# Kernel tuning notes

Hardware: AMD Instinct MI355X
Metric: run time of the kernel (lower is better)

The kernel has to match this reference:

```python
import jax, jax.numpy as jnp
import numpy as np

EPS = 1e-5  # torch InstanceNorm1d default


def _instance_norm_lastdim(t):
    # torch InstanceNorm1d applied to (b*h, n, d): normalizes over last axis d
    # per (b, h, n) with biased variance, no affine.
    mu = jnp.mean(t, axis=-1, keepdims=True)
    var = jnp.var(t, axis=-1, keepdims=True)
    return (t - mu) * jax.lax.rsqrt(var + EPS)


def setup_inputs() -> dict:
    key = jax.random.key(0)
    k1, k2, k3, k4 = jax.random.split(key, 4)
    b, n, dim = 4, 8192, 128
    heads, dim_head = 8, 64
    inner = heads * dim_head
    x = jax.random.normal(k1, (b, n, dim), dtype=jnp.float32)
    # nn.Linear(dim, inner*3, bias=False): weight (out, in); we store transposed (in, out)
    w_qkv = jax.random.normal(k2, (dim, inner * 3), dtype=jnp.float32) * (1.0 / np.sqrt(dim))
    w_out = jax.random.normal(k3, (inner, dim), dtype=jnp.float32) * (1.0 / np.sqrt(inner))
    b_out = jax.random.normal(k4, (dim,), dtype=jnp.float32) * 0.01
    return {"x": x, "w_qkv": w_qkv, "w_out": w_out, "b_out": b_out}


def reference(x, w_qkv, w_out, b_out):
    b, n, _ = x.shape
    heads, dim_head = 8, 64
    qkv = x @ w_qkv  # (b, n, 3*inner)
    q, k, v = jnp.split(qkv, 3, axis=-1)

    def to_heads(t):
        return t.reshape(b, n, heads, dim_head).transpose(0, 2, 1, 3)  # b h n d

    q, k, v = to_heads(q), to_heads(k), to_heads(v)
    # galerkin: norm k and v (InstanceNorm over dim_head axis)
    k = _instance_norm_lastdim(k)
    v = _instance_norm_lastdim(v)
    dots = jnp.einsum('bhnd,bhne->bhde', k, v)      # K^T V, small (d x d)
    out = jnp.einsum('bhnd,bhde->bhne', q, dots) * (1.0 / n)
    out = out.transpose(0, 2, 1, 3).reshape(b, n, heads * dim_head)
    return out @ w_out + b_out
```

## Files before the change

kernel.cpp:

```cpp
#include <hip/hip_runtime.h>

#define NN 8192
#define DIM 128

typedef short short8 __attribute__((ext_vector_type(8)));
typedef float f32x4 __attribute__((ext_vector_type(4)));

__device__ __forceinline__ unsigned short f2bf(float f) {
  unsigned int u = __float_as_uint(f);
  u = (u + 0x7FFFu + ((u >> 16) & 1u)) >> 16;
  return (unsigned short)u;
}
__device__ __forceinline__ unsigned int cvtpk(float a, float b) {
  unsigned int r;
  asm("v_cvt_pk_bf16_f32 %0, %1, %2" : "=v"(r) : "v"(a), "v"(b));
  return r;
}
__device__ __forceinline__ void gll16(const void* gsrc, void* ldst) {
  __builtin_amdgcn_global_load_lds(
      (const __attribute__((address_space(1))) unsigned int*)gsrc,
      (__attribute__((address_space(3))) unsigned int*)ldst, 16, 0, 0);
}
#define BAR_LGKM()                                          \
  do {                                                      \
    asm volatile("s_waitcnt lgkmcnt(0)" ::: "memory");      \
    __builtin_amdgcn_sched_barrier(0);                      \
    __builtin_amdgcn_s_barrier();                           \
    __builtin_amdgcn_sched_barrier(0);                      \
  } while (0)
#define BAR_VM()                                            \
  do {                                                      \
    asm volatile("s_waitcnt vmcnt(0)" ::: "memory");        \
    __builtin_amdgcn_sched_barrier(0);                      \
    __builtin_amdgcn_s_barrier();                           \
    __builtin_amdgcn_sched_barrier(0);                      \
  } while (0)

__global__ __launch_bounds__(256) void prep_kernel(const float* __restrict__ x,
                                                   const float* __restrict__ wqkv,
                                                   unsigned char* __restrict__ ximg,
                                                   unsigned char* __restrict__ wimg,
                                                   float* __restrict__ dots) {
  __shared__ __align__(16) unsigned char wb[32768];
  const int t = threadIdx.x;
  const int bx = blockIdx.x;
  if (bx < 1024) {
#pragma unroll
    for (int rep = 0; rep < 2; ++rep) {
      const int idx = bx * 512 + rep * 256 + t;
      const int bt = idx >> 10;
      const int o = (idx & 1023) << 4;
      const int r = o >> 8;
      const int q0 = o & 255;
      const int c0 = (q0 ^ ((r & 7) << 4)) >> 1;
      const float* src = x + ((size_t)(bt >> 7) * NN + (size_t)(bt & 127) * 64 + r) * DIM + c0;
      const float4 v0 = *(const float4*)src;
      const float4 v1 = *(const float4*)(src + 4);
      uint4 u;
      u.x = cvtpk(v0.x, v0.y);
      u.y = cvtpk(v0.z, v0.w);
      u.z = cvtpk(v1.x, v1.y);
      u.w = cvtpk(v1.z, v1.w);
      *(uint4*)(ximg + (size_t)idx * 16) = u;
    }
  } else if (bx < 1032) {
    const int h = bx - 1024;
    const int k = t >> 1;
    const int chalf = t & 1;
    const float* wp = wqkv + (size_t)k * 1536 + (chalf ? (1024 + h * 64) : (512 + h * 64));
    const float4* wp4 = (const float4*)wp;
    const int c0 = chalf * 64;
    float4 wv[16];
    float sum = 0.f;
#pragma unroll
    for (int jj = 0; jj < 16; ++jj) {
      wv[jj] = wp4[jj];
      sum += wv[jj].x + wv[jj].y + wv[jj].z + wv[jj].w;
    }
    const float mean = sum * (1.f / 64.f);
#pragma unroll
    for (int jj = 0; jj < 16; ++jj) {
      const int c = c0 + jj * 4;
      const unsigned int cx0 = (unsigned int)((c + 0) & 7) << 4;
      const unsigned int cx1 = (unsigned int)((c + 1) & 7) << 4;
      const unsigned int cx2 = (unsigned int)((c + 2) & 7) << 4;
      const unsigned int cx3 = (unsigned int)((c + 3) & 7) << 4;
      *(unsigned short*)(wb + (c + 0) * 256 + (((unsigned)(2 * k)) ^ cx0)) = f2bf(wv[jj].x - mean);
      *(unsigned short*)(wb + (c + 1) * 256 + (((unsigned)(2 * k)) ^ cx1)) = f2bf(wv[jj].y - mean);
      *(unsigned short*)(wb + (c + 2) * 256 + (((unsigned)(2 * k)) ^ cx2)) = f2bf(wv[jj].z - mean);
      *(unsigned short*)(wb + (c + 3) * 256 + (((unsigned)(2 * k)) ^ cx3)) = f2bf(wv[jj].w - mean);
    }
    __syncthreads();
    const uint4* s4 = (const uint4*)(wb + t * 128);
    uint4* d4 = (uint4*)(wimg + (size_t)h * 32768 + t * 128);
#pragma unroll
    for (int i = 0; i < 8; ++i) d4[i] = s4[i];
  } else {
    const int zb = bx - 1032;
    float4* dz = (float4*)dots + (size_t)zb * 4096 + t;
    const float4 z = make_float4(0.f, 0.f, 0.f, 0.f);
#pragma unroll
    for (int i = 0; i < 16; ++i) dz[i * 256] = z;
  }
}

__global__ __launch_bounds__(256, 3) void kv_dots_v5(const unsigned char* __restrict__ ximg,
                                                     const unsigned char* __restrict__ wimg,
                                                     float* __restrict__ dots) {
  __shared__ __align__(16) unsigned char smem[49152];
  unsigned char* const WB = smem;

  const int t = threadIdx.x;
  const int bx = blockIdx.x;
  const int h = bx >> 7;
  const int p = bx & 127;
  const int b = p >> 5;
  const int chunk = p & 31;

  const int wave = t >> 6;
  const int lane = t & 63;
  const int lb = lane & 15;
  const int kg = lane >> 4;
  const int g = wave & 1;
  const int ch = wave >> 1;
  const unsigned int lxor = (unsigned int)(lb & 7) << 4;
  const unsigned int rxor = (unsigned int)(lb & 3) << 4;

  const unsigned char* wsrc = wimg + (size_t)h * 32768;
  const unsigned char* xsrc = ximg + (size_t)(b * 128 + chunk * 4) * 16384;

#pragma unroll
  for (int i = 0; i < 8; ++i)
    gll16(wsrc + (i * 4 + wave) * 1024 + lane * 16, WB + (i * 4 + wave) * 1024);

  const int rrow = 16 * g + lb;
  short8 xf[4];
#pragma unroll
  for (int ks = 0; ks < 4; ++ks)
    xf[ks] = *(const short8*)(xsrc + rrow * 256 + (((unsigned)(ks * 64 + kg * 16)) ^ lxor));

  f32x4 dacc[4];
#pragma unroll
  for (int et = 0; et < 4; ++et) dacc[et] = (f32x4)0.f;

  BAR_VM();

  for (int tile = 0; tile < 8; ++tile) {
    short8 xn[4];
    if (tile < 7) {
      const unsigned char* tb = xsrc + (size_t)((tile + 1) >> 1) * 16384 + (size_t)((tile + 1) & 1) * 8192;
#pragma unroll
      for (int ks = 0; ks < 4; ++ks)
        xn[ks] = *(const short8*)(tb + rrow * 256 + (((unsigned)(ks * 64 + kg * 16)) ^ lxor));
    }

    f32x4 acc[4];
#pragma unroll
    for (int ct = 0; ct < 4; ++ct) acc[ct] = (f32x4)0.f;
#pragma unroll
    for (int ks = 0; ks < 4; ++ks) {
      const unsigned int koff = ((unsigned)(ks * 64 + kg * 16)) ^ lxor;
#pragma unroll
      for (int ct = 0; ct < 4; ++ct) {
        const short8 bf = *(const short8*)(WB + (ch * 64 + ct * 16 + lb) * 256 + koff);
        acc[ct] = __builtin_amdgcn_mfma_f32_16x16x32_bf16(xf[ks], bf, acc[ct], 0, 0, 0);
      }
    }

    float sc[4];
#pragma unroll
    for (int e = 0; e < 4; ++e) {
      float s = acc[0][e] * acc[0][e] + acc[1][e] * acc[1][e] +
                acc[2][e] * acc[2][e] + acc[3][e] * acc[3][e];
      s += __shfl_xor(s, 1);
      s += __shfl_xor(s, 2);
      s += __shfl_xor(s, 4);
      s += __shfl_xor(s, 8);
      sc[e] = rsqrtf(s * (1.f / 64.f) + 1e-5f);
    }

    unsigned char* const BUF = smem + 32768 + (tile & 1) * 8192;
    {
      unsigned char* const MYT = BUF + ch * 4096;
      const unsigned int rb = ((unsigned)(g * 32 + kg * 8)) ^ rxor;
#pragma unroll
      for (int ct = 0; ct < 4; ++ct) {
        uint2 w2;
        w2.x = cvtpk(acc[ct][0] * sc[0], acc[ct][1] * sc[1]);
        w2.y = cvtpk(acc[ct][2] * sc[2], acc[ct][3] * sc[3]);
        *(uint2*)(MYT + (ct * 16 + lb) * 64 + rb) = w2;
      }
    }
    BAR_LGKM();

    {
      const unsigned int soff = ((unsigned)(kg * 16)) ^ rxor;
      const short8 a = *(const short8*)(BUF + (wave * 16 + lb) * 64 + soff);
#pragma unroll
      for (int et = 0; et < 4; ++et) {
        const short8 bf = *(const short8*)(BUF + 4096 + (et * 16 + lb) * 64 + soff);
        dacc[et] = __builtin_amdgcn_mfma_f32_16x16x32_bf16(a, bf, dacc[et], 0, 0, 0);
      }
    }

#pragma unroll
    for (int ks = 0; ks < 4; ++ks) xf[ks] = xn[ks];
  }

  float* dp = dots + (size_t)(b * 8 + h) * 4096;
#pragma unroll
  for (int et = 0; et < 4; ++et) {
#pragma unroll
    for (int reg = 0; reg < 4; ++reg) {
      const int d = wave * 16 + kg * 4 + reg;
      const int e = et * 16 + lb;
      atomicAdd(&dp[d * 64 + e], dacc[et][reg]);
    }
  }
}

template <int TR>
__global__ __launch_bounds__(256) void tw_kernel(const float* __restrict__ wqkv,
                                                 const float* __restrict__ wout,
                                                 const float* __restrict__ dots,
                                                 float* __restrict__ part) {
  __shared__ __align__(16) float ds[64 * 66];
  __shared__ __align__(16) float wqT[64 * 36];
  __shared__ __align__(16) float Ts[32 * 66];
  __shared__ __align__(16) float wos[64 * 132];

  const int blk = blockIdx.x;
  const int bh = blk >> 2;
  const int cq = blk & 3;
  const int h = bh & 7;
  const int t = threadIdx.x;

  for (int i = t; i < 4096; i += 256)
    ds[(i >> 6) * 66 + (i & 63)] = dots[(size_t)bh * 4096 + i];

  for (int i = t; i < 2048; i += 256) {
    const int d = i >> 5;
    const int c = i & 31;
    wqT[d * 36 + c] = wqkv[(size_t)(cq * 32 + c) * 1536 + h * 64 + d];
  }

  for (int i = t; i < 2048; i += 256) {
    const int e = i >> 5;
    const int jj = (i & 31) * 4;
    *(float4*)&wos[e * 132 + jj] = *(const float4*)(wout + (size_t)(h * 64 + e) * 128 + jj);
  }
  __syncthreads();

  {
    const int c = t >> 3;
    const int e0 = (t & 7) * 8;
    float acc[8];
#pragma unroll
    for (int q = 0; q < 8; ++q) acc[q] = 0.f;
    for (int d = 0; d < 64; ++d) {
      const float wq = wqT[d * 36 + c];
      const float4 d0 = *(const float4*)&ds[d * 66 + e0];
      const float4 d1 = *(const float4*)&ds[d * 66 + e0 + 4];
      acc[0] += wq * d0.x; acc[1] += wq * d0.y; acc[2] += wq * d0.z; acc[3] += wq * d0.w;
      acc[4] += wq * d1.x; acc[5] += wq * d1.y; acc[6] += wq * d1.z; acc[7] += wq * d1.w;
    }
    *(float4*)&Ts[c * 66 + e0] = make_float4(acc[0], acc[1], acc[2], acc[3]);
    *(float4*)&Ts[c * 66 + e0 + 4] = make_float4(acc[4], acc[5], acc[6], acc[7]);
  }
  __syncthreads();

  {
    const int c = t >> 3;
    const int j0 = (t & 7) * 16;
    float acc[16];
#pragma unroll
    for (int q = 0; q < 16; ++q) acc[q] = 0.f;
    for (int e = 0; e < 64; ++e) {
      const float tv = Ts[c * 66 + e];
#pragma unroll
      for (int q = 0; q < 16; q += 4) {
        const float4 wv = *(const float4*)&wos[e * 132 + j0 + q];
        acc[q + 0] += tv * wv.x;
        acc[q + 1] += tv * wv.y;
        acc[q + 2] += tv * wv.z;
        acc[q + 3] += tv * wv.w;
      }
    }
    if (TR) {
      float* pp = part + (size_t)bh * 16384;
      const int cc = cq * 32 + c;
#pragma unroll
      for (int q = 0; q < 16; ++q) pp[(j0 + q) * 128 + cc] = acc[q];
    } else {
      float* pp = part + (size_t)bh * 16384 + (size_t)(cq * 32 + c) * 128 + j0;
#pragma unroll
      for (int q = 0; q < 16; q += 4)
        *(float4*)&pp[q] = make_float4(acc[q], acc[q + 1], acc[q + 2], acc[q + 3]);
    }
  }
}

__global__ __launch_bounds__(256) void bigw_reduce_v2(const float* __restrict__ part,
                                                      unsigned char* __restrict__ bigwimg) {
  const int idx = blockIdx.x * 256 + threadIdx.x;
  const int b = idx >> 11;
  const int o = (idx & 2047) << 4;
  const int j = o >> 8;
  const int q0 = o & 255;
  const int c0 = (q0 ^ ((j & 7) << 4)) >> 1;
  float s[8];
#pragma unroll
  for (int i = 0; i < 8; ++i) s[i] = 0.f;
  const float* pb = part + (size_t)b * 8 * 16384 + j * 128 + c0;
#pragma unroll
  for (int hh = 0; hh < 8; ++hh) {
    const float4 p0 = *(const float4*)(pb + hh * 16384);
    const float4 p1 = *(const float4*)(pb + hh * 16384 + 4);
    s[0] += p0.x; s[1] += p0.y; s[2] += p0.z; s[3] += p0.w;
    s[4] += p1.x; s[5] += p1.y; s[6] += p1.z; s[7] += p1.w;
  }
  const float inv_n = 1.f / (float)NN;
  uint4 u;
  u.x = cvtpk(s[0] * inv_n, s[1] * inv_n);
  u.y = cvtpk(s[2] * inv_n, s[3] * inv_n);
  u.z = cvtpk(s[4] * inv_n, s[5] * inv_n);
  u.w = cvtpk(s[6] * inv_n, s[7] * inv_n);
  *(uint4*)(bigwimg + (size_t)idx * 16) = u;
}

__global__ __launch_bounds__(256) void out_v2(const unsigned char* __restrict__ ximg,
                                              const unsigned char* __restrict__ bigwimg,
                                              const float* __restrict__ bout,
                                              float* __restrict__ out) {
  __shared__ __align__(16) unsigned char smem[49152];
  unsigned char* const XB = smem;
  unsigned char* const WJ = smem + 16384;

  const int t = threadIdx.x;
  const int bx = blockIdx.x;
  const int b = bx >> 7;
  const int tile = bx & 127;

  const int wave = t >> 6;
  const int lane = t & 63;
  const int lb = lane & 15;
  const int kg = lane >> 4;
  const unsigned int lxor = (unsigned int)(lb & 7) << 4;

  const unsigned char* wsrc = bigwimg + (size_t)b * 32768;
  const unsigned char* xsrc = ximg + (size_t)(b * 128 + tile) * 16384;

#pragma unroll
  for (int i = 0; i < 8; ++i)
    gll16(wsrc + (wave * 8 + i) * 1024 + lane * 16, WJ + (wave * 8 + i) * 1024);
#pragma unroll
  for (int i = 0; i < 4; ++i)
    gll16(xsrc + (wave * 4 + i) * 1024 + lane * 16, XB + (wave * 4 + i) * 1024);

  float bias[8];
#pragma unroll
  for (int ct = 0; ct < 8; ++ct) bias[ct] = bout[ct * 16 + lb];

  BAR_VM();

  f32x4 acc[8];
#pragma unroll
  for (int ct = 0; ct < 8; ++ct) acc[ct] = (f32x4)0.f;
  const int arow = wave * 16 + lb;
#pragma unroll
  for (int ks = 0; ks < 4; ++ks) {
    const unsigned int koff = (unsigned int)(ks * 64 + kg * 16);
    const short8 a = *(const short8*)(XB + arow * 256 + (koff ^ lxor));
#pragma unroll
    for (int ct = 0; ct < 8; ++ct) {
      const short8 bf = *(const short8*)(WJ + (ct * 16 + lb) * 256 + (koff ^ lxor));
      acc[ct] = __builtin_amdgcn_mfma_f32_16x16x32_bf16(a, bf, acc[ct], 0, 0, 0);
    }
  }

  float* op = out + (size_t)(b * NN + tile * 64 + 16 * wave + kg * 4) * DIM;
#pragma unroll
  for (int ct = 0; ct < 8; ++ct) {
#pragma unroll
    for (int reg = 0; reg < 4; ++reg) {
      op[reg * DIM + ct * 16 + lb] = acc[ct][reg] + bias[ct];
    }
  }
}

__global__ __launch_bounds__(256) void zero_dots_fb(float* __restrict__ dots) {
  float4* dz = (float4*)dots + (size_t)blockIdx.x * 4096 + threadIdx.x;
  const float4 z = make_float4(0.f, 0.f, 0.f, 0.f);
#pragma unroll
  for (int i = 0; i < 16; ++i) dz[i * 256] = z;
}

__global__ __launch_bounds__(256) void kv_dots_fb(const float* __restrict__ x,
                                                  const float* __restrict__ wqkv,
                                                  float* __restrict__ dots) {
  __shared__ __align__(16) unsigned char smem[49152];
  unsigned char* const XB = smem;
  unsigned char* const KT = smem;
  unsigned char* const VT = smem + 8192;
  unsigned char* const WB = smem + 16384;

  const int t = threadIdx.x;
  const int bx = blockIdx.x;
  const int h = bx >> 7;
  const int p = bx & 127;
  const int b = p >> 5;
  const int chunk = p & 31;
  const int row0 = chunk * 256;

  const int wave = t >> 6;
  const int lane = t & 63;
  const int lb = lane & 15;
  const int kg = lane >> 4;
  const unsigned int lxor = (unsigned int)(lb & 7) << 4;

  {
    const int k = t >> 1;
    const int chalf = t & 1;
    const float* wp = wqkv + (size_t)k * 1536 + (chalf ? (1024 + h * 64) : (512 + h * 64));
    const float4* wp4 = (const float4*)wp;
    const int c0 = chalf * 64;
    float4 wv[16];
    float sum = 0.f;
#pragma unroll
    for (int jj = 0; jj < 16; ++jj) {
      wv[jj] = wp4[jj];
      sum += wv[jj].x + wv[jj].y + wv[jj].z + wv[jj].w;
    }
    const float mean = sum * (1.f / 64.f);
#pragma unroll
    for (int jj = 0; jj < 16; ++jj) {
      const int c = c0 + jj * 4;
      const unsigned int cx0 = (unsigned int)((c + 0) & 7) << 4;
      const unsigned int cx1 = (unsigned int)((c + 1) & 7) << 4;
      const unsigned int cx2 = (unsigned int)((c + 2) & 7) << 4;
      const unsigned int cx3 = (unsigned int)((c + 3) & 7) << 4;
      *(unsigned short*)(WB + (c + 0) * 256 + (((unsigned)(2 * k)) ^ cx0)) = f2bf(wv[jj].x - mean);
      *(unsigned short*)(WB + (c + 1) * 256 + (((unsigned)(2 * k)) ^ cx1)) = f2bf(wv[jj].y - mean);
      *(unsigned short*)(WB + (c + 2) * 256 + (((unsigned)(2 * k)) ^ cx2)) = f2bf(wv[jj].z - mean);
      *(unsigned short*)(WB + (c + 3) * 256 + (((unsigned)(2 * k)) ^ cx3)) = f2bf(wv[jj].w - mean);
    }
  }

  f32x4 dacc[4];
#pragma unroll
  for (int nt = 0; nt < 4; ++nt) dacc[nt] = (f32x4)0.f;

  __syncthreads();

  for (int tile = 0; tile < 4; ++tile) {
    const int rowbase = row0 + tile * 64;
    __syncthreads();
    {
      const int r = t >> 2;
      const int cb = (t & 3) * 32;
      const float4* gp4 = (const float4*)(x + (size_t)(b * NN + rowbase + r) * DIM + cb);
      const unsigned int rxor = (unsigned int)(r & 7) << 4;
#pragma unroll
      for (int jj = 0; jj < 4; ++jj) {
        const float4 v0 = gp4[2 * jj];
        const float4 v1 = gp4[2 * jj + 1];
        uint4 u;
        u.x = cvtpk(v0.x, v0.y);
        u.y = cvtpk(v0.z, v0.w);
        u.z = cvtpk(v1.x, v1.y);
        u.w = cvtpk(v1.z, v1.w);
        *(uint4*)(XB + r * 256 + (((unsigned)(2 * cb + 16 * jj)) ^ rxor)) = u;
      }
    }
    __syncthreads();

    f32x4 acc[8];
#pragma unroll
    for (int ct = 0; ct < 8; ++ct) acc[ct] = (f32x4)0.f;
    const int arow = wave * 16 + lb;
#pragma unroll
    for (int ks = 0; ks < 4; ++ks) {
      const unsigned int koff = (unsigned int)(ks * 64 + kg * 16);
      const short8 a = *(const short8*)(XB + arow * 256 + (koff ^ lxor));
#pragma unroll
      for (int ct = 0; ct < 8; ++ct) {
        const short8 bf = *(const short8*)(WB + (ct * 16 + lb) * 256 + (koff ^ lxor));
        acc[ct] = __builtin_amdgcn_mfma_f32_16x16x32_bf16(a, bf, acc[ct], 0, 0, 0);
      }
    }

    float kscale[4];
#pragma unroll
    for (int e = 0; e < 4; ++e) {
      float sk = acc[0][e] * acc[0][e] + acc[1][e] * acc[1][e] +
                 acc[2][e] * acc[2][e] + acc[3][e] * acc[3][e];
      float sv = acc[4][e] * acc[4][e] + acc[5][e] * acc[5][e] +
                 acc[6][e] * acc[6][e] + acc[7][e] * acc[7][e];
      sk += __shfl_xor(sk, 1); sv += __shfl_xor(sv, 1);
      sk += __shfl_xor(sk, 2); sv += __shfl_xor(sv, 2);
      sk += __shfl_xor(sk, 4); sv += __shfl_xor(sv, 4);
      sk += __shfl_xor(sk, 8); sv += __shfl_xor(sv, 8);
      kscale[e] = rsqrtf(sk * (1.f / 64.f) + 1e-5f) * rsqrtf(sv * (1.f / 64.f) + 1e-5f);
    }

    __syncthreads();
    {
      const unsigned int rb2 = (unsigned int)(32 * wave + kg * 8);
#pragma unroll
      for (int ct = 0; ct < 4; ++ct) {
        uint2 w;
        w.x = cvtpk(acc[ct][0] * kscale[0], acc[ct][1] * kscale[1]);
        w.y = cvtpk(acc[ct][2] * kscale[2], acc[ct][3] * kscale[3]);
        *(uint2*)(KT + (ct * 16 + lb) * 128 + (rb2 ^ lxor)) = w;
      }
#pragma unroll
      for (int ct = 4; ct < 8; ++ct) {
        uint2 w;
        w.x = cvtpk(acc[ct][0], acc[ct][1]);
        w.y = cvtpk(acc[ct][2], acc[ct][3]);
        *(uint2*)(VT + ((ct - 4) * 16 + lb) * 128 + (rb2 ^ lxor)) = w;
      }
    }
    __syncthreads();

#pragma unroll
    for (int ks2 = 0; ks2 < 2; ++ks2) {
      const unsigned int koff = (unsigned int)(ks2 * 64 + kg * 16);
      const short8 a = *(const short8*)(KT + (wave * 16 + lb) * 128 + (koff ^ lxor));
#pragma unroll
      for (int nt = 0; nt < 4; ++nt) {
        const short8 bf = *(const short8*)(VT + (nt * 16 + lb) * 128 + (koff ^ lxor));
        dacc[nt] = __builtin_amdgcn_mfma_f32_16x16x32_bf16(a, bf, dacc[nt], 0, 0, 0);
      }
    }
  }

  float* dp = dots + (size_t)(b * 8 + h) * 4096;
#pragma unroll
  for (int nt = 0; nt < 4; ++nt) {
#pragma unroll
    for (int reg = 0; reg < 4; ++reg) {
      const int d = 16 * wave + kg * 4 + reg;
      const int e = nt * 16 + lb;
      atomicAdd(&dp[d * 64 + e], dacc[nt][reg]);
    }
  }
}

__global__ __launch_bounds__(256) void bigw_reduce_fb(const float* __restrict__ part,
                                                      float* __restrict__ bigw) {
  const int i = blockIdx.x * 256 + threadIdx.x;
  const int b = i >> 14;
  const int cj = i & 16383;
  const float* pp = part + (size_t)b * 8 * 16384 + cj;
  float s = 0.f;
#pragma unroll
  for (int h = 0; h < 8; ++h) s += pp[h * 16384];
  bigw[i] = s * (1.f / (float)NN);
}

__global__ __launch_bounds__(256) void out_fb(const float* __restrict__ x,
                                              const float* __restrict__ bigw,
                                              const float* __restrict__ bout,
                                              float* __restrict__ out) {
  __shared__ __align__(16) unsigned char smem[49152];
  unsigned char* const XB = smem;
  unsigned char* const WB = smem + 16384;

  const int t = threadIdx.x;
  const int bx = blockIdx.x;
  const int b = bx >> 7;
  const int rowbase = (bx & 127) * 64;

  const int wave = t >> 6;
  const int lane = t & 63;
  const int lb = lane & 15;
  const int kg = lane >> 4;
  const unsigned int lxor = (unsigned int)(lb & 7) << 4;

  {
    const int c = t >> 1;
    const int jhalf = t & 1;
    const float4* wp4 = (const float4*)(bigw + (size_t)b * 16384 + (size_t)c * 128 + jhalf * 64);
    const int j0 = jhalf * 64;
#pragma unroll
    for (int q = 0; q < 16; ++q) {
      const float4 v = wp4[q];
      const int j = j0 + q * 4;
      const unsigned int jx0 = (unsigned int)((j + 0) & 7) << 4;
      const unsigned int jx1 = (unsigned int)((j + 1) & 7) << 4;
      const unsigned int jx2 = (unsigned int)((j + 2) & 7) << 4;
      const unsigned int jx3 = (unsigned int)((j + 3) & 7) << 4;
      *(unsigned short*)(WB + (j + 0) * 256 + (((unsigned)(2 * c)) ^ jx0)) = f2bf(v.x);
      *(unsigned short*)(WB + (j + 1) * 256 + (((unsigned)(2 * c)) ^ jx1)) = f2bf(v.y);
      *(unsigned short*)(WB + (j + 2) * 256 + (((unsigned)(2 * c)) ^ jx2)) = f2bf(v.z);
      *(unsigned short*)(WB + (j + 3) * 256 + (((unsigned)(2 * c)) ^ jx3)) = f2bf(v.w);
    }
  }

  float bias[8];
#pragma unroll
  for (int ct = 0; ct < 8; ++ct) bias[ct] = bout[ct * 16 + lb];

  {
    const int r = t >> 2;
    const int cb = (t & 3) * 32;
    const float4* gp4 = (const float4*)(x + (size_t)(b * NN + rowbase + r) * DIM + cb);
    const unsigned int rxor = (unsigned int)(r & 7) << 4;
#pragma unroll
    for (int jj = 0; jj < 4; ++jj) {
      const float4 v0 = gp4[2 * jj];
      const float4 v1 = gp4[2 * jj + 1];
      uint4 u;
      u.x = cvtpk(v0.x, v0.y);
      u.y = cvtpk(v0.z, v0.w);
      u.z = cvtpk(v1.x, v1.y);
      u.w = cvtpk(v1.z, v1.w);
      *(uint4*)(XB + r * 256 + (((unsigned)(2 * cb + 16 * jj)) ^ rxor)) = u;
    }
  }
  __syncthreads();

  f32x4 acc[8];
#pragma unroll
  for (int ct = 0; ct < 8; ++ct) acc[ct] = (f32x4)0.f;
  const int arow = wave * 16 + lb;
#pragma unroll
  for (int ks = 0; ks < 4; ++ks) {
    const unsigned int koff = (unsigned int)(ks * 64 + kg * 16);
    const short8 a = *(const short8*)(XB + arow * 256 + (koff ^ lxor));
#pragma unroll
    for (int ct = 0; ct < 8; ++ct) {
      const short8 bf = *(const short8*)(WB + (ct * 16 + lb) * 256 + (koff ^ lxor));
      acc[ct] = __builtin_amdgcn_mfma_f32_16x16x32_bf16(a, bf, acc[ct], 0, 0, 0);
    }
  }

  float* op = out + (size_t)(b * NN + rowbase + 16 * wave + kg * 4) * DIM;
#pragma unroll
  for (int ct = 0; ct < 8; ++ct) {
#pragma unroll
    for (int reg = 0; reg < 4; ++reg) {
      op[reg * DIM + ct * 16 + lb] = acc[ct][reg] + bias[ct];
    }
  }
}

extern "C" void kernel_launch(void* const* d_in, const int* in_sizes, int n_in,
                              void* d_out, int out_size, void* d_ws, size_t ws_size,
                              hipStream_t stream) {
  (void)in_sizes; (void)n_in; (void)out_size;
  const float* x = (const float*)d_in[0];
  const float* wqkv = (const float*)d_in[1];
  const float* wout = (const float*)d_in[2];
  const float* bout = (const float*)d_in[3];
  float* out = (float*)d_out;

  const size_t NEED = 8388608ull + 262144ull + 131072ull + 524288ull + 2097152ull;
  if (ws_size >= NEED) {
    unsigned char* ximg = (unsigned char*)d_ws;
    unsigned char* wimg = ximg + 8388608;
    unsigned char* bigwimg = wimg + 262144;
    float* dots = (float*)(bigwimg + 131072);
    float* part = dots + 131072;

    hipLaunchKernelGGL(prep_kernel, dim3(1040), dim3(256), 0, stream, x, wqkv, ximg, wimg, dots);
    hipLaunchKernelGGL(kv_dots_v5, dim3(1024), dim3(256), 0, stream, ximg, wimg, dots);
    hipLaunchKernelGGL((tw_kernel<1>), dim3(128), dim3(256), 0, stream, wqkv, wout, dots, part);
    hipLaunchKernelGGL(bigw_reduce_v2, dim3(32), dim3(256), 0, stream, part, bigwimg);
    hipLaunchKernelGGL(out_v2, dim3(512), dim3(256), 0, stream, ximg, bigwimg, bout, out);
  } else {
    float* dots = (float*)d_ws;
    float* part = dots + 131072;
    float* bigw = part + 524288;
    hipLaunchKernelGGL(zero_dots_fb, dim3(8), dim3(256), 0, stream, dots);
    hipLaunchKernelGGL(kv_dots_fb, dim3(1024), dim3(256), 0, stream, x, wqkv, dots);
    hipLaunchKernelGGL((tw_kernel<0>), dim3(128), dim3(256), 0, stream, wqkv, wout, dots, part);
    hipLaunchKernelGGL(bigw_reduce_fb, dim3(256), dim3(256), 0, stream, part, bigw);
    hipLaunchKernelGGL(out_fb, dim3(512), dim3(256), 0, stream, x, bigw, bout, out);
  }
}
```

Measured before the change: 66.34 us.

## Drop bf16 x image; convert fp32 x in registers inside consumers

Removes the prep pass that converted x to a swizzled bf16 workspace image. kv_dots and out kernels now load fp32 x directly and convert to bf16 in registers before MFMA. This eliminates a write of the bf16 image and its re-reads, plus shrinks the prep launch, at the cost of reading fp32 x (double bytes) in kv_dots, which re-reads it across 8 heads, and in the out kernel.

New measurement: 76.13 us. +14.8%, slower.

```diff
diff --git a/kernel.cpp b/kernel.cpp
--- a/kernel.cpp
+++ b/kernel.cpp
@@ -15,6 +15,14 @@
   unsigned int r;
   asm("v_cvt_pk_bf16_f32 %0, %1, %2" : "=v"(r) : "v"(a), "v"(b));
   return r;
+}
+__device__ __forceinline__ short8 cvt8(const float4 a, const float4 b) {
+  union { uint4 u; short8 s; } r;
+  r.u.x = cvtpk(a.x, a.y);
+  r.u.y = cvtpk(a.z, a.w);
+  r.u.z = cvtpk(b.x, b.y);
+  r.u.w = cvtpk(b.z, b.w);
+  return r.s;
 }
 __device__ __forceinline__ void gll16(const void* gsrc, void* ldst) {
   __builtin_amdgcn_global_load_lds(
@@ -36,35 +44,14 @@
     __builtin_amdgcn_sched_barrier(0);                      \
   } while (0)
 
-__global__ __launch_bounds__(256) void prep_kernel(const float* __restrict__ x,
-                                                   const float* __restrict__ wqkv,
-                                                   unsigned char* __restrict__ ximg,
-                                                   unsigned char* __restrict__ wimg,
-                                                   float* __restrict__ dots) {
+__global__ __launch_bounds__(256) void prep2_kernel(const float* __restrict__ wqkv,
+                                                    unsigned char* __restrict__ wimg,
+                                                    float* __restrict__ dots) {
   __shared__ __align__(16) unsigned char wb[32768];
   const int t = threadIdx.x;
   const int bx = blockIdx.x;
-  if (bx < 1024) {
-#pragma unroll
-    for (int rep = 0; rep < 2; ++rep) {
-      const int idx = bx * 512 + rep * 256 + t;
-      const int bt = idx >> 10;
-      const int o = (idx & 1023) << 4;
-      const int r = o >> 8;
-      const int q0 = o & 255;
-      const int c0 = (q0 ^ ((r & 7) << 4)) >> 1;
-      const float* src = x + ((size_t)(bt >> 7) * NN + (size_t)(bt & 127) * 64 + r) * DIM + c0;
-      const float4 v0 = *(const float4*)src;
-      const float4 v1 = *(const float4*)(src + 4);
-      uint4 u;
-      u.x = cvtpk(v0.x, v0.y);
-      u.y = cvtpk(v0.z, v0.w);
-      u.z = cvtpk(v1.x, v1.y);
-      u.w = cvtpk(v1.z, v1.w);
-      *(uint4*)(ximg + (size_t)idx * 16) = u;
-    }
-  } else if (bx < 1032) {
-    const int h = bx - 1024;
+  if (bx < 8) {
+    const int h = bx;
     const int k = t >> 1;
     const int chalf = t & 1;
     const float* wp = wqkv + (size_t)k * 1536 + (chalf ? (1024 + h * 64) : (512 + h * 64));
@@ -96,7 +83,7 @@
 #pragma unroll
     for (int i = 0; i < 8; ++i) d4[i] = s4[i];
   } else {
-    const int zb = bx - 1032;
+    const int zb = bx - 8;
     float4* dz = (float4*)dots + (size_t)zb * 4096 + t;
     const float4 z = make_float4(0.f, 0.f, 0.f, 0.f);
 #pragma unroll
@@ -104,7 +91,7 @@
   }
 }
 
-__global__ __launch_bounds__(256, 3) void kv_dots_v5(const unsigned char* __restrict__ ximg,
+__global__ __launch_bounds__(256, 3) void kv_dots_v6(const float* __restrict__ x,
                                                      const unsigned char* __restrict__ wimg,
                                                      float* __restrict__ dots) {
   __shared__ __align__(16) unsigned char smem[49152];
@@ -123,21 +110,22 @@
   const int kg = lane >> 4;
   const int g = wave & 1;
   const int ch = wave >> 1;
-  const unsigned int lxor = (unsigned int)(lb & 7) << 4;
   const unsigned int rxor = (unsigned int)(lb & 3) << 4;
 
   const unsigned char* wsrc = wimg + (size_t)h * 32768;
-  const unsigned char* xsrc = ximg + (size_t)(b * 128 + chunk * 4) * 16384;
+  const float* xbase = x + ((size_t)b * NN + (size_t)chunk * 256 + 16 * g + lb) * DIM + kg * 8;
 
 #pragma unroll
   for (int i = 0; i < 8; ++i)
     gll16(wsrc + (i * 4 + wave) * 1024 + lane * 16, WB + (i * 4 + wave) * 1024);
 
-  const int rrow = 16 * g + lb;
   short8 xf[4];
 #pragma unroll
-  for (int ks = 0; ks < 4; ++ks)
-    xf[ks] = *(const short8*)(xsrc + rrow * 256 + (((unsigned)(ks * 64 + kg * 16)) ^ lxor));
+  for (int ks = 0; ks < 4; ++ks) {
+    const float4 a = *(const float4*)(xbase + ks * 32);
+    const float4 c = *(const float4*)(xbase + ks * 32 + 4);
+    xf[ks] = cvt8(a, c);
+  }
 
   f32x4 dacc[4];
 #pragma unroll
@@ -145,13 +133,17 @@
 
   BAR_VM();
 
+  const unsigned int lxor = (unsigned int)(lb & 7) << 4;
+
   for (int tile = 0; tile < 8; ++tile) {
-    short8 xn[4];
+    float4 xnr[8];
     if (tile < 7) {
-      const unsigned char* tb = xsrc + (size_t)((tile + 1) >> 1) * 16384 + (size_t)((tile + 1) & 1) * 8192;
-#pragma unroll
-      for (int ks = 0; ks < 4; ++ks)
-        xn[ks] = *(const short8*)(tb + rrow * 256 + (((unsigned)(ks * 64 + kg * 16)) ^ lxor));
+      const float* tb = xbase + (size_t)(tile + 1) * 32 * DIM;
+#pragma unroll
+      for (int ks = 0; ks < 4; ++ks) {
+        xnr[2 * ks] = *(const float4*)(tb + ks * 32);
+        xnr[2 * ks + 1] = *(const float4*)(tb + ks * 32 + 4);
+      }
     }
 
     f32x4 acc[4];
@@ -204,7 +196,7 @@
     }
 
 #pragma unroll
-    for (int ks = 0; ks < 4; ++ks) xf[ks] = xn[ks];
+    for (int ks = 0; ks < 4; ++ks) xf[ks] = cvt8(xnr[2 * ks], xnr[2 * ks + 1]);
   }
 
   float* dp = dots + (size_t)(b * 8 + h) * 4096;
@@ -328,13 +320,11 @@
   *(uint4*)(bigwimg + (size_t)idx * 16) = u;
 }
 
-__global__ __launch_bounds__(256) void out_v2(const unsigned char* __restrict__ ximg,
+__global__ __launch_bounds__(256) void out_v4(const float* __restrict__ x,
                                               const unsigned char* __restrict__ bigwimg,
                                               const float* __restrict__ bout,
                                               float* __restrict__ out) {
-  __shared__ __align__(16) unsigned char smem[49152];
-  unsigned char* const XB = smem;
-  unsigned char* const WJ = smem + 16384;
+  __shared__ __align__(16) unsigned char WJ[32768];
 
   const int t = threadIdx.x;
   const int bx = blockIdx.x;
@@ -348,14 +338,18 @@
   const unsigned int lxor = (unsigned int)(lb & 7) << 4;
 
   const unsigned char* wsrc = bigwimg + (size_t)b * 32768;
-  const unsigned char* xsrc = ximg + (size_t)(b * 128 + tile) * 16384;
-
 #pragma unroll
   for (int i = 0; i < 8; ++i)
     gll16(wsrc + (wave * 8 + i) * 1024 + lane * 16, WJ + (wave * 8 + i) * 1024);
-#pragma unroll
-  for (int i = 0; i < 4; ++i)
-    gll16(xsrc + (wave * 4 + i) * 1024 + lane * 16, XB + (wave * 4 + i) * 1024);
+
+  const float* xb = x + ((size_t)b * NN + (size_t)tile * 64 + wave * 16 + lb) * DIM + kg * 8;
+  short8 af[4];
+#pragma unroll
+  for (int ks = 0; ks < 4; ++ks) {
+    const float4 a = *(const float4*)(xb + ks * 32);
+    const float4 c = *(const float4*)(xb + ks * 32 + 4);
+    af[ks] = cvt8(a, c);
+  }
 
   float bias[8];
 #pragma unroll
@@ -366,19 +360,17 @@
   f32x4 acc[8];
 #pragma unroll
   for (int ct = 0; ct < 8; ++ct) acc[ct] = (f32x4)0.f;
-  const int arow = wave * 16 + lb;
 #pragma unroll
   for (int ks = 0; ks < 4; ++ks) {
     const unsigned int koff = (unsigned int)(ks * 64 + kg * 16);
-    const short8 a = *(const short8*)(XB + arow * 256 + (koff ^ lxor));
 #pragma unroll
     for (int ct = 0; ct < 8; ++ct) {
       const short8 bf = *(const short8*)(WJ + (ct * 16 + lb) * 256 + (koff ^ lxor));
-      acc[ct] = __builtin_amdgcn_mfma_f32_16x16x32_bf16(a, bf, acc[ct], 0, 0, 0);
-    }
-  }
-
-  float* op = out + (size_t)(b * NN + tile * 64 + 16 * wave + kg * 4) * DIM;
+      acc[ct] = __builtin_amdgcn_mfma_f32_16x16x32_bf16(af[ks], bf, acc[ct], 0, 0, 0);
+    }
+  }
+
+  float* op = out + ((size_t)b * NN + (size_t)tile * 64 + 16 * wave + kg * 4) * DIM;
 #pragma unroll
   for (int ct = 0; ct < 8; ++ct) {
 #pragma unroll
@@ -656,19 +648,18 @@
   const float* bout = (const float*)d_in[3];
   float* out = (float*)d_out;
 
-  const size_t NEED = 8388608ull + 262144ull + 131072ull + 524288ull + 2097152ull;
+  const size_t NEED = 262144ull + 131072ull + 524288ull + 2097152ull;
   if (ws_size >= NEED) {
-    unsigned char* ximg = (unsigned char*)d_ws;
-    unsigned char* wimg = ximg + 8388608;
+    unsigned char* wimg = (unsigned char*)d_ws;
     unsigned char* bigwimg = wimg + 262144;
     float* dots = (float*)(bigwimg + 131072);
     float* part = dots + 131072;
 
-    hipLaunchKernelGGL(prep_kernel, dim3(1040), dim3(256), 0, stream, x, wqkv, ximg, wimg, dots);
-    hipLaunchKernelGGL(kv_dots_v5, dim3(1024), dim3(256), 0, stream, ximg, wimg, dots);
+    hipLaunchKernelGGL(prep2_kernel, dim3(16), dim3(256), 0, stream, wqkv, wimg, dots);
+    hipLaunchKernelGGL(kv_dots_v6, dim3(1024), dim3(256), 0, stream, x, wimg, dots);
     hipLaunchKernelGGL((tw_kernel<1>), dim3(128), dim3(256), 0, stream, wqkv, wout, dots, part);
     hipLaunchKernelGGL(bigw_reduce_v2, dim3(32), dim3(256), 0, stream, part, bigwimg);
-    hipLaunchKernelGGL(out_v2, dim3(512), dim3(256), 0, stream, ximg, bigwimg, bout, out);
+    hipLaunchKernelGGL(out_v4, dim3(512), dim3(256), 0, stream, x, bigwimg, bout, out);
   } else {
     float* dots = (float*)d_ws;
     float* part = dots + 131072;
```
